# Performance work log

Measured on AMD Instinct MI355X. Metric: run time of the kernel, lower is better.

The kernel has to match this reference:

```python
import jax, jax.numpy as jnp
import numpy as np

NUM_LABELS = 64
START, END, PAD = 0, 1, 2
B, L, V, D = 128, 1024, 30000, 256


def make_transitions(key):
    # replicates CRF.init_weights
    t = jax.random.uniform(key, (NUM_LABELS, NUM_LABELS), minval=-0.1, maxval=0.1)
    t = t.at[:, START].set(-10000.0)
    t = t.at[END, :].set(-10000.0)
    t = t.at[PAD, :].set(-10000.0)
    t = t.at[:, PAD].set(-10000.0)
    t = t.at[PAD, PAD].set(0.0)
    t = t.at[PAD, END].set(0.0)
    return t.astype(jnp.float32)


def setup_inputs() -> dict:
    key = jax.random.key(0)
    k0, k1, k2, k3, k4 = jax.random.split(key, 5)
    x = jax.random.randint(k0, (B, L), 0, V)
    tags = jax.random.randint(k1, (B, L), 0, NUM_LABELS)
    mask = jnp.ones((B, L), dtype=jnp.float32)  # ignored by CRF (source passes mask=None)
    embed = jax.random.normal(k2, (V, D), dtype=jnp.float32)
    W = jax.random.normal(k3, (D, NUM_LABELS), dtype=jnp.float32) * 0.05
    b = jnp.zeros((NUM_LABELS,), dtype=jnp.float32)
    trans = make_transitions(k4)
    return {"x": x, "tags": tags, "mask": mask, "embed": embed, "W": W, "b": b, "trans": trans}


def _crf_nll(emissions, tags, trans):
    # emissions: [B, L, T]; tags: [B, L]; trans: [T, T]
    # NOTE: original CRF.forward ignores the user mask (passes mask=None ->
    # all-ones mask), so every position is valid and last tag is tags[:, -1].
    # gold path score
    e_scores = jnp.take_along_axis(emissions, tags[:, :, None], axis=2)[:, :, 0].sum(axis=1)
    t_scores = trans[tags[:, :-1], tags[:, 1:]].sum(axis=1)
    scores = e_scores + t_scores + trans[START, tags[:, 0]] + trans[tags[:, -1], END]
    # log partition: forward algorithm (log-space recursion over time)
    alpha0 = trans[START][None, :] + emissions[:, 0]  # [B, T]

    def step(alphas, emit_t):
        # alphas: [B, T_prev] -> logsumexp over previous tag
        new = jax.nn.logsumexp(alphas[:, :, None] + trans[None, :, :], axis=1) + emit_t
        return new, None

    alphas, _ = jax.lax.scan(step, alpha0, jnp.swapaxes(emissions[:, 1:], 0, 1))
    log_z = jax.nn.logsumexp(alphas + trans[:, END][None, :], axis=1)  # [B]
    return -jnp.sum(scores - log_z)


def reference(x, tags, mask, embed, W, b, trans):
    emissions = embed[x] @ W + b  # [B, L, T]
    return _crf_nll(emissions, tags, trans)
```

## Files before the change

kernel.cpp:

```cpp
#include <hip/hip_runtime.h>
#include <hip/hip_bf16.h>

#define B_ 128
#define L_ 1024
#define T_ 64
#define CSH 5
#define C_ 32

using short8 = __attribute__((ext_vector_type(8))) short;
using f32x4  = __attribute__((ext_vector_type(4))) float;
using f32x16 = __attribute__((ext_vector_type(16))) float;

static __device__ __forceinline__ unsigned short bfb(float x) {
  return __builtin_bit_cast(unsigned short, __float2bfloat16(x));
}
static __device__ __forceinline__ float asf(unsigned u) { return __builtin_bit_cast(float, u); }
static __device__ __forceinline__ float bf2f(unsigned short b) { return asf(((unsigned)b) << 16); }
static __device__ __forceinline__ unsigned pk2(float lo, float hi) {
  __hip_bfloat162 h = __float22bfloat162_rn(float2{lo, hi});
  unsigned u;
  __builtin_memcpy(&u, &h, 4);
  return u;
}
static __device__ __forceinline__ unsigned pk2t(float lo, float hi) {
  return __builtin_amdgcn_perm(__builtin_bit_cast(unsigned, hi),
                               __builtin_bit_cast(unsigned, lo), 0x07060302u);
}
static __device__ __forceinline__ void pswap(unsigned& x, unsigned& y) {
  asm("v_permlane32_swap_b32 %0, %1" : "+v"(x), "+v"(y));
}

__global__ __launch_bounds__(256) void k_scan(const int* __restrict__ x,
                                              const int* __restrict__ tags,
                                              const float* __restrict__ embed,
                                              const float* __restrict__ W,
                                              const float* __restrict__ bias,
                                              const float* __restrict__ trans,
                                              unsigned short* __restrict__ XT,
                                              float* __restrict__ rlog,
                                              float* __restrict__ goldF) {
  __shared__ unsigned short Wsw[16384];
  __shared__ __align__(16) unsigned short Ftile[4][2048];
  for (int e = threadIdx.x; e < 16384; e += 256) {
    int k = e >> 6, n = e & 63;
    int idx = ((k >> 5) << 11) + ((n >> 4) << 9) + (((k >> 3) & 3) << 7) + ((n & 15) << 3) + (k & 7);
    Wsw[idx] = bfb(W[e]);
  }
  __syncthreads();

  const int wv = threadIdx.x >> 6, L = threadIdx.x & 63;
  const int job = blockIdx.x * 4 + wv;
  const int c = job & (C_ - 1);
  const int b = job >> CSH;
  const int K = (1023 + C_ - 1) >> CSH;
  const int a = 1 + c * K;
  const int len = min(K, 1024 - a);
  const int nh = L & 31, hh = L >> 5;
  const int m = L & 15, q = L >> 4;
  unsigned short* Ft = Ftile[wv];

  const float bj0 = bias[m], bj1 = bias[16 + m], bj2 = bias[32 + m], bj3 = bias[48 + m];
  for (int p = 0; p < 2; p++) {
    int tok = a + 16 * p + m;
    if (tok > 1023) tok = 1023;
    const float* er = embed + (size_t)x[b * 1024 + tok] * 256;
    f32x4 acc[4] = {{0.f,0.f,0.f,0.f},{0.f,0.f,0.f,0.f},{0.f,0.f,0.f,0.f},{0.f,0.f,0.f,0.f}};
#pragma unroll
    for (int kap = 0; kap < 8; kap++) {
      float4 p0 = *(const float4*)(er + 32 * kap + 8 * q);
      float4 p1 = *(const float4*)(er + 32 * kap + 8 * q + 4);
      unsigned u0 = pk2(p0.x, p0.y), u1 = pk2(p0.z, p0.w);
      unsigned u2 = pk2(p1.x, p1.y), u3 = pk2(p1.z, p1.w);
      short8 af = __builtin_bit_cast(short8, make_uint4(u0, u1, u2, u3));
#pragma unroll
      for (int u = 0; u < 4; u++) {
        short8 bf8 = *(const short8*)&Wsw[kap * 2048 + u * 512 + q * 128 + m * 8];
        acc[u] = __builtin_amdgcn_mfma_f32_16x16x32_bf16(af, bf8, acc[u], 0, 0, 0);
      }
    }
#pragma unroll
    for (int r = 0; r < 4; r++) {
      float e0 = acc[0][r] + bj0, e1 = acc[1][r] + bj1;
      float e2 = acc[2][r] + bj2, e3 = acc[3][r] + bj3;
      float mr = fmaxf(fmaxf(e0, e1), fmaxf(e2, e3));
#pragma unroll
      for (int off = 1; off < 16; off <<= 1) mr = fmaxf(mr, __shfl_xor(mr, off));
      float x0 = __expf(e0 - mr), x1 = __expf(e1 - mr);
      float x2 = __expf(e2 - mr), x3 = __expf(e3 - mr);
      float sr = (x0 + x1) + (x2 + x3);
#pragma unroll
      for (int off = 1; off < 16; off <<= 1) sr += __shfl_xor(sr, off);
      float rs = 1.0f / sr;
      const int row = 16 * p + 4 * q + r;
      Ft[row * 64 + m]      = bfb(x0 * rs);
      Ft[row * 64 + 16 + m] = bfb(x1 * rs);
      Ft[row * 64 + 32 + m] = bfb(x2 * rs);
      Ft[row * 64 + 48 + m] = bfb(x3 * rs);
    }
  }
  if (L < len) {
    const int tgv = tags[b * 1024 + a + L];
    goldF[b * 1024 + a + L] = __logf(bf2f(Ft[L * 64 + tgv]));
  }

  short8 Af[2][4];
#pragma unroll
  for (int I = 0; I < 2; I++)
#pragma unroll
    for (int kap = 0; kap < 4; kap++) {
      short8 aa;
#pragma unroll
      for (int d = 0; d < 8; d++) {
        const int k = 16 * kap + 8 * hh + d;
        aa[d] = (short)bfb(__expf(trans[k * T_ + 32 * I + nh]));
      }
      Af[I][kap] = aa;
    }

  unsigned Bf[4][2][4];
#pragma unroll
  for (int kap = 0; kap < 4; kap++)
#pragma unroll
    for (int J = 0; J < 2; J++)
#pragma unroll
      for (int dw = 0; dw < 4; dw++) {
        int k0 = 16 * kap + 8 * hh + 2 * dw, n = 32 * J + nh;
        unsigned u = 0;
        if (k0 == n) u = 0x3F80u;
        if (k0 + 1 == n) u = 0x3F800000u;
        Bf[kap][J][dw] = u;
      }

  float logacc = 0.f;
  const f32x16 Z = {};

  for (int s = 0; s < len; s++) {
    uint2 Fc[2][4];
#pragma unroll
    for (int I = 0; I < 2; I++)
#pragma unroll
      for (int j = 0; j < 4; j++)
        Fc[I][j] = *(const uint2*)&Ft[s * 64 + (16 * I + 4 * j + 2 * hh) * 2];
    const bool rn = ((s & 15) == 15);
    float rs = 1.0f;
#pragma unroll
    for (int J = 0; J < 2; J++) {
      f32x16 D[2];
#pragma unroll
      for (int I = 0; I < 2; I++) {
        short8 b0 = __builtin_bit_cast(short8,
            make_uint4(Bf[0][J][0], Bf[0][J][1], Bf[0][J][2], Bf[0][J][3]));
        f32x16 d = __builtin_amdgcn_mfma_f32_32x32x16_bf16(Af[I][0], b0, Z, 0, 0, 0);
#pragma unroll
        for (int kap = 1; kap < 4; kap++) {
          short8 bk = __builtin_bit_cast(short8,
              make_uint4(Bf[kap][J][0], Bf[kap][J][1], Bf[kap][J][2], Bf[kap][J][3]));
          d = __builtin_amdgcn_mfma_f32_32x32x16_bf16(Af[I][kap], bk, d, 0, 0, 0);
        }
        D[I] = d;
      }
#pragma unroll
      for (int I = 0; I < 2; I++)
#pragma unroll
        for (int j = 0; j < 4; j++) {
          uint2 g = Fc[I][j];
          float f0 = asf(g.x << 16), f1 = asf(g.x & 0xffff0000u);
          float f2 = asf(g.y << 16), f3 = asf(g.y & 0xffff0000u);
          D[I][4 * j + 0] *= f0;
          D[I][4 * j + 1] *= f1;
          D[I][4 * j + 2] *= f2;
          D[I][4 * j + 3] *= f3;
        }
      if (rn) {
        if (J == 0) {
          float mx = D[0][0];
#pragma unroll
          for (int I = 0; I < 2; I++)
#pragma unroll
            for (int r = 0; r < 16; r++) mx = fmaxf(mx, D[I][r]);
#pragma unroll
          for (int off = 1; off < 64; off <<= 1) mx = fmaxf(mx, __shfl_xor(mx, off));
          rs = 1.0f / mx;
          logacc += __logf(mx);
        }
#pragma unroll
        for (int I = 0; I < 2; I++)
#pragma unroll
          for (int r = 0; r < 16; r++) D[I][r] *= rs;
      }
      unsigned PDt[2][4][2];
#pragma unroll
      for (int I = 0; I < 2; I++)
#pragma unroll
        for (int j = 0; j < 4; j++) {
          PDt[I][j][0] = pk2t(D[I][4 * j + 0], D[I][4 * j + 1]);
          PDt[I][j][1] = pk2t(D[I][4 * j + 2], D[I][4 * j + 3]);
        }
      if (s == len - 1) {
        unsigned short* Xrow = XT + (size_t)job * 4096 + 32 * J + nh;
#pragma unroll
        for (int I = 0; I < 2; I++)
#pragma unroll
          for (int j = 0; j < 4; j++)
#pragma unroll
            for (int pp = 0; pp < 2; pp++) {
              const int r = 32 * I + 8 * j + 4 * hh + 2 * pp;
              Xrow[(size_t)r * 64] = (unsigned short)(PDt[I][j][pp] & 0xffffu);
              Xrow[(size_t)(r + 1) * 64] = (unsigned short)(PDt[I][j][pp] >> 16);
            }
      } else {
#pragma unroll
        for (int kap = 0; kap < 4; kap++) {
          const int Ip = kap >> 1, e2 = 2 * (kap & 1);
          unsigned x0 = PDt[Ip][e2][0], y0 = PDt[Ip][e2 + 1][0];
          unsigned x1 = PDt[Ip][e2][1], y1 = PDt[Ip][e2 + 1][1];
          pswap(x0, y0);
          pswap(x1, y1);
          Bf[kap][J][0] = x0;
          Bf[kap][J][1] = x1;
          Bf[kap][J][2] = y0;
          Bf[kap][J][3] = y1;
        }
      }
    }
  }
  if (L == 0) rlog[job] = logacc;
}

__global__ __launch_bounds__(256) void k_apply(const unsigned short* __restrict__ XT,
                                               const float* __restrict__ rlog,
                                               const float* __restrict__ goldF,
                                               const int* __restrict__ x,
                                               const float* __restrict__ embed,
                                               const float* __restrict__ W,
                                               const float* __restrict__ bias,
                                               const float* __restrict__ trans,
                                               const int* __restrict__ tags,
                                               float* __restrict__ out) {
  const int b = blockIdx.x, tid = threadIdx.x;
  __shared__ float sred[4];
  __shared__ __align__(16) float vS[64];
  const int* tg = tags + (size_t)b * L_;
  float acc = 0.f;
  for (int l = tid; l < L_; l += 256) {
    if (l > 0) acc += goldF[(size_t)b * L_ + l];
    if (l < L_ - 1) acc += trans[tg[l] * T_ + tg[l + 1]];
  }
#pragma unroll
  for (int off = 32; off > 0; off >>= 1) acc += __shfl_xor(acc, off);
  if ((tid & 63) == 0) sred[tid >> 6] = acc;
  __syncthreads();
  if (tid >= 64) return;
  const int i = tid;
  float score = (sred[0] + sred[1]) + (sred[2] + sred[3]);
  const float* er0 = embed + (size_t)x[(size_t)b * L_] * 256;
  float e = bias[i];
#pragma unroll 8
  for (int d = 0; d < 256; d++) e = fmaf(er0[d], W[d * T_ + i], e);
  float mr = e;
#pragma unroll
  for (int off = 1; off < 64; off <<= 1) mr = fmaxf(mr, __shfl_xor(mr, off));
  float pex = __expf(e - mr);
  float sr = pex;
#pragma unroll
  for (int off = 1; off < 64; off <<= 1) sr += __shfl_xor(sr, off);
  const int t0 = tg[0];
  score += (__shfl(e, t0) - mr) - __logf(sr);
  score += trans[t0] + trans[tg[L_ - 1] * T_ + 1];
  float v = __expf(trans[i]) * (pex / sr);
  float lacc = 0.f;
  vS[i] = v;
  const uint4* Xb = (const uint4*)XT + (size_t)b * C_ * 512;
  uint4 Xr[8];
#pragma unroll
  for (int t = 0; t < 8; t++) Xr[t] = Xb[i * 8 + t];
  for (int c = 0; c < C_; c++) {
    uint4 Xn[8];
    if (c + 1 < C_) {
#pragma unroll
      for (int t = 0; t < 8; t++) Xn[t] = Xb[(size_t)(c + 1) * 512 + i * 8 + t];
    }
    float nv = 0.f;
#pragma unroll
    for (int t = 0; t < 8; t++) {
      float4 va = *(const float4*)&vS[8 * t];
      float4 vb = *(const float4*)&vS[8 * t + 4];
      nv = fmaf(asf(Xr[t].x << 16), va.x, nv);
      nv = fmaf(asf(Xr[t].x & 0xffff0000u), va.y, nv);
      nv = fmaf(asf(Xr[t].y << 16), va.z, nv);
      nv = fmaf(asf(Xr[t].y & 0xffff0000u), va.w, nv);
      nv = fmaf(asf(Xr[t].z << 16), vb.x, nv);
      nv = fmaf(asf(Xr[t].z & 0xffff0000u), vb.y, nv);
      nv = fmaf(asf(Xr[t].w << 16), vb.z, nv);
      nv = fmaf(asf(Xr[t].w & 0xffff0000u), vb.w, nv);
    }
    float mx = nv;
#pragma unroll
    for (int off = 1; off < 64; off <<= 1) mx = fmaxf(mx, __shfl_xor(mx, off));
    v = nv * (1.0f / mx);
    lacc += __logf(mx) + rlog[b * C_ + c];
    vS[i] = v;
#pragma unroll
    for (int t = 0; t < 8; t++) Xr[t] = Xn[t];
  }
  float t2 = v * __expf(trans[i * T_ + 1]);
#pragma unroll
  for (int off = 1; off < 64; off <<= 1) t2 += __shfl_xor(t2, off);
  if (i == 0) {
    const float logz = lacc + __logf(t2);
    atomicAdd(out, -(score - logz));
  }
}

extern "C" void kernel_launch(void* const* d_in, const int* in_sizes, int n_in,
                              void* d_out, int out_size, void* d_ws, size_t ws_size,
                              hipStream_t stream) {
  const int* x = (const int*)d_in[0];
  const int* tags = (const int*)d_in[1];
  const float* embed = (const float*)d_in[3];
  const float* W = (const float*)d_in[4];
  const float* bias = (const float*)d_in[5];
  const float* trans = (const float*)d_in[6];

  char* ws = (char*)d_ws;
  unsigned short* XT = (unsigned short*)ws;
  float* rlog = (float*)(ws + (size_t)C_ * 1048576);
  float* goldF = (float*)((char*)rlog + (size_t)128 * C_ * 4);
  float* out = (float*)d_out;

  hipMemsetAsync(out, 0, sizeof(float), stream);
  k_scan<<<32 * C_, 256, 0, stream>>>(x, tags, embed, W, bias, trans, XT, rlog, goldF);
  k_apply<<<B_, 256, 0, stream>>>(XT, rlog, goldF, x, embed, W, bias, trans, tags, out);
}
```

Before: 210.1 us.

## Precompute swizzled bf16 W in prep kernel, read from global in scan

New measurement: 255.8 us. 1.22x slower.

```diff
diff --git a/kernel.cpp b/kernel.cpp
--- a/kernel.cpp
+++ b/kernel.cpp
@@ -30,24 +30,31 @@
   asm("v_permlane32_swap_b32 %0, %1" : "+v"(x), "+v"(y));
 }
 
-__global__ __launch_bounds__(256) void k_scan(const int* __restrict__ x,
-                                              const int* __restrict__ tags,
-                                              const float* __restrict__ embed,
-                                              const float* __restrict__ W,
-                                              const float* __restrict__ bias,
-                                              const float* __restrict__ trans,
-                                              unsigned short* __restrict__ XT,
-                                              float* __restrict__ rlog,
-                                              float* __restrict__ goldF) {
-  __shared__ unsigned short Wsw[16384];
+__global__ __launch_bounds__(256) void k_prep(const float* __restrict__ W,
+                                              unsigned short* __restrict__ Wswz,
+                                              float* __restrict__ out) {
+  if (blockIdx.x == 0 && threadIdx.x == 0) out[0] = 0.f;
+  const int t = blockIdx.x * 256 + threadIdx.x;
+  const int e = t * 4, k = e >> 6, n0 = e & 63;
+  float4 w4 = *(const float4*)(W + e);
+  const int base = ((k >> 5) << 11) + ((n0 >> 4) << 9) + (((k >> 3) & 3) << 7) +
+                   ((n0 & 15) << 3) + (k & 7);
+  Wswz[base + 0]  = bfb(w4.x);
+  Wswz[base + 8]  = bfb(w4.y);
+  Wswz[base + 16] = bfb(w4.z);
+  Wswz[base + 24] = bfb(w4.w);
+}
+
+__global__ __launch_bounds__(256, 4) void k_scan(const int* __restrict__ x,
+                                                 const int* __restrict__ tags,
+                                                 const float* __restrict__ embed,
+                                                 const unsigned short* __restrict__ Wswz,
+                                                 const float* __restrict__ bias,
+                                                 const float* __restrict__ trans,
+                                                 unsigned short* __restrict__ XT,
+                                                 float* __restrict__ rlog,
+                                                 float* __restrict__ goldF) {
   __shared__ __align__(16) unsigned short Ftile[4][2048];
-  for (int e = threadIdx.x; e < 16384; e += 256) {
-    int k = e >> 6, n = e & 63;
-    int idx = ((k >> 5) << 11) + ((n >> 4) << 9) + (((k >> 3) & 3) << 7) + ((n & 15) << 3) + (k & 7);
-    Wsw[idx] = bfb(W[e]);
-  }
-  __syncthreads();
-
   const int wv = threadIdx.x >> 6, L = threadIdx.x & 63;
   const int job = blockIdx.x * 4 + wv;
   const int c = job & (C_ - 1);
@@ -74,7 +81,7 @@
       short8 af = __builtin_bit_cast(short8, make_uint4(u0, u1, u2, u3));
 #pragma unroll
       for (int u = 0; u < 4; u++) {
-        short8 bf8 = *(const short8*)&Wsw[kap * 2048 + u * 512 + q * 128 + m * 8];
+        short8 bf8 = *(const short8*)&Wswz[kap * 2048 + u * 512 + q * 128 + m * 8];
         acc[u] = __builtin_amdgcn_mfma_f32_16x16x32_bf16(af, bf8, acc[u], 0, 0, 0);
       }
     }
@@ -326,9 +333,10 @@
   unsigned short* XT = (unsigned short*)ws;
   float* rlog = (float*)(ws + (size_t)C_ * 1048576);
   float* goldF = (float*)((char*)rlog + (size_t)128 * C_ * 4);
+  unsigned short* Wswz = (unsigned short*)((char*)goldF + (size_t)B_ * L_ * 4);
   float* out = (float*)d_out;
 
-  hipMemsetAsync(out, 0, sizeof(float), stream);
-  k_scan<<<32 * C_, 256, 0, stream>>>(x, tags, embed, W, bias, trans, XT, rlog, goldF);
+  k_prep<<<16, 256, 0, stream>>>(W, Wswz, out);
+  k_scan<<<32 * C_, 256, 0, stream>>>(x, tags, embed, Wswz, bias, trans, XT, rlog, goldF);
   k_apply<<<B_, 256, 0, stream>>>(XT, rlog, goldF, x, embed, W, bias, trans, tags, out);
 }
```
